# Optimization experiments

Hardware: AMD Instinct MI355X
Metric: run time of the kernel (lower is better)

## Reference

```python
import jax, jax.numpy as jnp
import numpy as np

B, T, H, OUT_STEPS, D = 131072, 51, 64, 20, 4


def setup_inputs() -> dict:
    key = jax.random.key(0)
    ks = jax.random.split(key, 11)
    s = 1.0 / np.sqrt(H)  # torch nn.GRU / nn.Linear uniform init bound
    u = lambda k, shape: jax.random.uniform(k, shape, jnp.float32, -s, s)
    return {
        "input_seq": jax.random.normal(ks[0], (B, T, D), jnp.float32),
        "enc_Wih": u(ks[1], (3 * H, D)),
        "enc_Whh": u(ks[2], (3 * H, H)),
        "enc_bih": u(ks[3], (3 * H,)),
        "enc_bhh": u(ks[4], (3 * H,)),
        "dec_Wih": u(ks[5], (3 * H, D)),
        "dec_Whh": u(ks[6], (3 * H, H)),
        "dec_bih": u(ks[7], (3 * H,)),
        "dec_bhh": u(ks[8], (3 * H,)),
        "lin_W": u(ks[9], (D, H)),
        "lin_b": u(ks[10], (D,)),
    }


def _gru_cell(x, h, Wih, Whh, bih, bhh):
    """PyTorch GRU cell semantics. x: [B,D_in], h: [B,H]."""
    gi = x @ Wih.T + bih  # [B,3H]
    gh = h @ Whh.T + bhh  # [B,3H]
    ir, iz, inn = jnp.split(gi, 3, axis=-1)
    hr, hz, hn = jnp.split(gh, 3, axis=-1)
    r = jax.nn.sigmoid(ir + hr)
    z = jax.nn.sigmoid(iz + hz)
    n = jnp.tanh(inn + r * hn)
    return (1.0 - z) * n + z * h


def reference(input_seq, enc_Wih, enc_Whh, enc_bih, enc_bhh,
              dec_Wih, dec_Whh, dec_bih, dec_bhh, lin_W, lin_b):
    # offset: last observed point, broadcast over the 20 output steps
    offset = input_seq[:, -1:, :]  # [B,1,D]
    diffs = input_seq[:, 1:] - input_seq[:, :-1]  # [B,T-1,D]; dropout p=0 -> identity
    h0 = jnp.zeros((input_seq.shape[0], H), input_seq.dtype)

    def enc_step(h, x_t):
        return _gru_cell(x_t, h, enc_Wih, enc_Whh, enc_bih, enc_bhh), None

    hn, _ = jax.lax.scan(enc_step, h0, jnp.swapaxes(diffs, 0, 1))  # final hidden [B,H]

    def dec_step(carry, _):
        h, px = carry
        h = _gru_cell(px, h, dec_Wih, dec_Whh, dec_bih, dec_bhh)
        x = h @ lin_W.T + lin_b + px  # linear + residual
        return (h, x), x

    _, xs = jax.lax.scan(dec_step, (hn, diffs[:, -1]), None, length=OUT_STEPS)
    out = jnp.swapaxes(xs, 0, 1)  # [B,OUT_STEPS,D]
    return out + offset
```

## Files before the change

kernel.cpp:

```cpp
#include <hip/hip_runtime.h>

namespace {

constexpr int kT = 51;
constexpr int kOut = 20;
constexpr float kL2E  = 1.4426950408889634f;
constexpr float kL2E2 = 2.8853900817779268f;

typedef __attribute__((ext_vector_type(8))) short bf16x8;
typedef __attribute__((ext_vector_type(4))) float f32x4;
typedef __attribute__((ext_vector_type(2))) float f32x2;

union FragU {
    bf16x8 v;
    unsigned long long u64[2];
    unsigned int u32[4];
    unsigned short s[8];
};

__device__ __forceinline__ unsigned short f2bf(float x) {
    union { float f; unsigned int u; } v;
    v.f = x;
    unsigned int r = (v.u + 0x7fffu + ((v.u >> 16) & 1u)) >> 16;
    return (unsigned short)r;
}

__device__ __forceinline__ unsigned int packbf(float a, float b) {
    union { float f; unsigned int u; } ua, ub;
    ua.f = a; ub.f = b;
    return __builtin_amdgcn_perm(ub.u + 0x8000u, ua.u + 0x8000u, 0x07060302u);
}

__global__ __launch_bounds__(256, 2) void gru_encdec(
    const float* __restrict__ input,
    const float* __restrict__ eWih, const float* __restrict__ eWhh,
    const float* __restrict__ ebih, const float* __restrict__ ebhh,
    const float* __restrict__ dWih, const float* __restrict__ dWhh,
    const float* __restrict__ dbih, const float* __restrict__ dbhh,
    const float* __restrict__ linW, const float* __restrict__ linb,
    float* __restrict__ out)
{
    __shared__ __align__(16) unsigned short hbuf[2][4][16 * 68];

    const int lane = (int)(threadIdx.x & 63u);
    const int w = (int)(threadIdx.x >> 6u);
    const int q = lane >> 4;
    const int i = lane & 15;
    const bool q0 = (q == 0);
    const long bb = (long)blockIdx.x * 64 + i;

    const float* xrow[4];
#pragma unroll
    for (int g = 0; g < 4; ++g) xrow[g] = input + (bb + 16 * g) * (kT * 4);

    bf16x8 WA[3][2];
    bf16x8 WAUG[3];
    f32x4 bhhn4;
    float hp[4][4];
    bf16x8 bh[4][2];
    float px[4][4];
    const f32x4 z4 = {0.f, 0.f, 0.f, 0.f};
    const bf16x8 zfr = {0, 0, 0, 0, 0, 0, 0, 0};

    auto load_whh = [&](const float* __restrict__ Whh) {
#pragma unroll
        for (int l = 0; l < 3; ++l) {
            const int tau = 4 * l + w;
            const float sc = (l < 2) ? kL2E : kL2E2;
#pragma unroll
            for (int f = 0; f < 2; ++f) {
                const float* ptr = Whh + (tau * 16 + i) * 64 + f * 32 + q * 8;
                FragU fu;
#pragma unroll
                for (int j = 0; j < 8; ++j) fu.s[j] = f2bf(ptr[j] * sc);
                WA[l][f] = fu.v;
            }
        }
    };

    auto load_aug = [&](const float* __restrict__ Wih,
                        const float* __restrict__ bih,
                        const float* __restrict__ bhh) {
#pragma unroll
        for (int l = 0; l < 3; ++l) {
            const int tau = 4 * l + w;
            const float sc = (l < 2) ? kL2E : kL2E2;
            FragU fu;
            fu.u64[0] = 0; fu.u64[1] = 0;
            if (q0) {
                int j = tau * 16 + i;
#pragma unroll
                for (int d = 0; d < 4; ++d) fu.s[d] = f2bf(Wih[j * 4 + d] * sc);
                float bias = (l < 2) ? (bih[j] + bhh[j]) : bih[j];
                fu.s[4] = f2bf(bias * sc);
            }
            WAUG[l] = fu.v;
        }
#pragma unroll
        for (int r = 0; r < 4; ++r)
            bhhn4[r] = bhh[128 + 16 * w + 4 * q + r] * kL2E2;
    };

    auto make_baug = [&](const float* pxv) -> bf16x8 {
        FragU fu;
        fu.u32[0] = packbf(pxv[0], pxv[1]);
        fu.u32[1] = packbf(pxv[2], pxv[3]);
        fu.u32[2] = 0x3f80u;
        fu.u32[3] = 0u;
        return fu.v;
    };

    auto gru_step = [&](int ssel, const bf16x8* ba) {
#pragma unroll
        for (int p = 0; p < 2; ++p) {
            const int g0 = 2 * p, g1 = 2 * p + 1;
            f32x4 R[2], Z[2], Ni[2], Nh[2];
#pragma unroll
            for (int k = 0; k < 2; ++k) {
                const int g = 2 * p + k;
                R[k] = __builtin_amdgcn_mfma_f32_16x16x32_bf16(WAUG[0], ba[g], z4, 0, 0, 0);
                R[k] = __builtin_amdgcn_mfma_f32_16x16x32_bf16(WA[0][0], bh[g][0], R[k], 0, 0, 0);
                R[k] = __builtin_amdgcn_mfma_f32_16x16x32_bf16(WA[0][1], bh[g][1], R[k], 0, 0, 0);
                Z[k] = __builtin_amdgcn_mfma_f32_16x16x32_bf16(WAUG[1], ba[g], z4, 0, 0, 0);
                Z[k] = __builtin_amdgcn_mfma_f32_16x16x32_bf16(WA[1][0], bh[g][0], Z[k], 0, 0, 0);
                Z[k] = __builtin_amdgcn_mfma_f32_16x16x32_bf16(WA[1][1], bh[g][1], Z[k], 0, 0, 0);
                Ni[k] = __builtin_amdgcn_mfma_f32_16x16x32_bf16(WAUG[2], ba[g], z4, 0, 0, 0);
                Nh[k] = __builtin_amdgcn_mfma_f32_16x16x32_bf16(WA[2][0], bh[g][0], bhhn4, 0, 0, 0);
                Nh[k] = __builtin_amdgcn_mfma_f32_16x16x32_bf16(WA[2][1], bh[g][1], Nh[k], 0, 0, 0);
            }
            float hva[4], hvb[4];
            const f32x2 one = {1.f, 1.f};
            const f32x2 m2 = {-2.f, -2.f};
#pragma unroll
            for (int r = 0; r < 4; ++r) {
                f32x2 a = { __builtin_amdgcn_exp2f(-R[0][r]),
                            __builtin_amdgcn_exp2f(-R[1][r]) };
                f32x2 c = { __builtin_amdgcn_exp2f(-Z[0][r]),
                            __builtin_amdgcn_exp2f(-Z[1][r]) };
                f32x2 A = a + one, C = c + one;
                f32x2 P = A * C;
                float rpp = __builtin_amdgcn_rcpf(P.x * P.y);
                f32x2 Ps = {P.y, P.x};
                f32x2 rp = rpp * Ps;
                f32x2 rr = rp * C;
                f32x2 zz = rp * A;
                f32x2 Nh2 = {Nh[0][r], Nh[1][r]};
                f32x2 Ni2 = {Ni[0][r], Ni[1][r]};
                f32x2 p2 = __builtin_elementwise_fma(rr, Nh2, Ni2);
                f32x2 E = { __builtin_amdgcn_exp2f(p2.x),
                            __builtin_amdgcn_exp2f(p2.y) };
                f32x2 D = E + one;
                float rdd = __builtin_amdgcn_rcpf(D.x * D.y);
                f32x2 Ds = {D.y, D.x};
                f32x2 t = rdd * Ds;
                f32x2 n = __builtin_elementwise_fma(t, m2, one);
                f32x2 h = {hp[g0][r], hp[g1][r]};
                f32x2 hv = __builtin_elementwise_fma(zz, h - n, n);
                hp[g0][r] = hv.x; hp[g1][r] = hv.y;
                hva[r] = hv.x;    hvb[r] = hv.y;
            }
            uint2 wva, wvb;
            wva.x = packbf(hva[0], hva[1]); wva.y = packbf(hva[2], hva[3]);
            wvb.x = packbf(hvb[0], hvb[1]); wvb.y = packbf(hvb[2], hvb[3]);
            *(uint2*)&hbuf[ssel][g0][i * 68 + 16 * w + 4 * q] = wva;
            *(uint2*)&hbuf[ssel][g1][i * 68 + 16 * w + 4 * q] = wvb;
        }
        __syncthreads();
#pragma unroll
        for (int g = 0; g < 4; ++g) {
            const unsigned short* hw = hbuf[ssel][g];
            FragU fA, fB;
            fA.u64[0] = *(const unsigned long long*)&hw[i * 68 + 8 * q];
            fA.u64[1] = *(const unsigned long long*)&hw[i * 68 + 8 * q + 4];
            fB.u64[0] = *(const unsigned long long*)&hw[i * 68 + 32 + 8 * q];
            fB.u64[1] = *(const unsigned long long*)&hw[i * 68 + 32 + 8 * q + 4];
            bh[g][0] = fA.v;
            bh[g][1] = fB.v;
        }
    };

#pragma unroll
    for (int g = 0; g < 4; ++g) {
#pragma unroll
        for (int r = 0; r < 4; ++r) hp[g][r] = 0.f;
        bh[g][0] = zfr;
        bh[g][1] = zfr;
    }
    load_whh(eWhh);
    load_aug(eWih, ebih, ebhh);

    float4 xp[4], xn[4];
#pragma unroll
    for (int g = 0; g < 4; ++g) {
        xp[g] = *(const float4*)(xrow[g]);
        xn[g] = *(const float4*)(xrow[g] + 4);
    }
    bf16x8 ba[4];
#pragma unroll 2
    for (int s = 0; s < kT - 1; ++s) {
#pragma unroll
        for (int g = 0; g < 4; ++g) {
            px[g][0] = xn[g].x - xp[g].x; px[g][1] = xn[g].y - xp[g].y;
            px[g][2] = xn[g].z - xp[g].z; px[g][3] = xn[g].w - xp[g].w;
            xp[g] = xn[g];
        }
        int idx = s + 2; if (idx > kT - 1) idx = kT - 1;
#pragma unroll
        for (int g = 0; g < 4; ++g)
            xn[g] = *(const float4*)(xrow[g] + idx * 4);
#pragma unroll
        for (int g = 0; g < 4; ++g) ba[g] = make_baug(px[g]);
        gru_step(s & 1, ba);
    }
    float4 off[4];
#pragma unroll
    for (int g = 0; g < 4; ++g) off[g] = xp[g];

    load_whh(dWhh);
    load_aug(dWih, dbih, dbhh);

    bf16x8 AL0, AL1, AL2;
    {
        FragU a0, a1, a2;
        a0.u64[0] = a0.u64[1] = 0;
        a1.u64[0] = a1.u64[1] = 0;
        a2.u64[0] = a2.u64[1] = 0;
        if (i < 4) {
            const float* p0 = linW + i * 64 + q * 8;
            const float* p1 = linW + i * 64 + 32 + q * 8;
#pragma unroll
            for (int j = 0; j < 8; ++j) {
                a0.s[j] = f2bf(p0[j]);
                a1.s[j] = f2bf(p1[j]);
            }
            if (q0) a2.s[4] = f2bf(linb[i]);
        }
        AL0 = a0.v; AL1 = a1.v; AL2 = a2.v;
    }

#pragma unroll 2
    for (int s = 0; s < kOut; ++s) {
#pragma unroll
        for (int g = 0; g < 4; ++g) ba[g] = make_baug(px[g]);
        gru_step(s & 1, ba);
#pragma unroll
        for (int g = 0; g < 4; ++g) {
            f32x4 X = __builtin_amdgcn_mfma_f32_16x16x32_bf16(AL2, ba[g], z4, 0, 0, 0);
            X = __builtin_amdgcn_mfma_f32_16x16x32_bf16(AL0, bh[g][0], X, 0, 0, 0);
            X = __builtin_amdgcn_mfma_f32_16x16x32_bf16(AL1, bh[g][1], X, 0, 0, 0);
            px[g][0] += X[0]; px[g][1] += X[1];
            px[g][2] += X[2]; px[g][3] += X[3];
        }
#pragma unroll
        for (int g = 0; g < 4; ++g) {
            if (w == g && q0) {
                float* op = out + (bb + 16 * g) * (kOut * 4) + s * 4;
                float4 v;
                v.x = px[g][0] + off[g].x; v.y = px[g][1] + off[g].y;
                v.z = px[g][2] + off[g].z; v.w = px[g][3] + off[g].w;
                *(float4*)op = v;
            }
        }
    }
}

}

extern "C" void kernel_launch(void* const* d_in, const int* in_sizes, int n_in,
                              void* d_out, int out_size, void* d_ws, size_t ws_size,
                              hipStream_t stream) {
    const float* input = (const float*)d_in[0];
    const float* eWih = (const float*)d_in[1];
    const float* eWhh = (const float*)d_in[2];
    const float* ebih = (const float*)d_in[3];
    const float* ebhh = (const float*)d_in[4];
    const float* dWih = (const float*)d_in[5];
    const float* dWhh = (const float*)d_in[6];
    const float* dbih = (const float*)d_in[7];
    const float* dbhh = (const float*)d_in[8];
    const float* linW = (const float*)d_in[9];
    const float* linb = (const float*)d_in[10];
    float* out = (float*)d_out;

    const int B = in_sizes[0] / (kT * 4);
    const int nblocks = B / 64;
    gru_encdec<<<nblocks, 256, 0, stream>>>(input, eWih, eWhh, ebih, ebhh,
                                            dWih, dWhh, dbih, dbhh,
                                            linW, linb, out);
}
```

Measured before the change: 639.1 us.

## Give each wave its own 16 sequences and keep hidden state in registers

Work is now split by sequence instead of by gate rows: each wave owns 16 batch rows and holds all three gates' weight tiles (12x2 fragments), so it computes every hidden unit itself. The Whh rows are permuted so that the MFMA output layout matches the B-operand layout of the next step. The new hidden state can then be packed straight into bh0/bh1 with no LDS round trip or __syncthreads per timestep. The cost is much higher VGPR use for weights, which with launch_bounds(256,2) may cause spills or lower occupancy, and there are fewer independent MFMA chains per wave to hide latency.

```diff
diff --git a/kernel.cpp b/kernel.cpp
--- a/kernel.cpp
+++ b/kernel.cpp
@@ -40,40 +40,38 @@
     const float* __restrict__ linW, const float* __restrict__ linb,
     float* __restrict__ out)
 {
-    __shared__ __align__(16) unsigned short hbuf[2][4][16 * 68];
-
     const int lane = (int)(threadIdx.x & 63u);
     const int w = (int)(threadIdx.x >> 6u);
     const int q = lane >> 4;
     const int i = lane & 15;
     const bool q0 = (q == 0);
-    const long bb = (long)blockIdx.x * 64 + i;
-
-    const float* xrow[4];
-#pragma unroll
-    for (int g = 0; g < 4; ++g) xrow[g] = input + (bb + 16 * g) * (kT * 4);
-
-    bf16x8 WA[3][2];
-    bf16x8 WAUG[3];
-    f32x4 bhhn4;
+    const long bb = ((long)blockIdx.x * 4 + w) * 16 + i;
+    const float* __restrict__ xrow = input + bb * (kT * 4);
+    const int ibase = 8 * (i >> 2) + (i & 3);
+
+    bf16x8 WA[3][4][2];
+    bf16x8 WAUG[3][4];
+    f32x4 bhhn[4];
     float hp[4][4];
-    bf16x8 bh[4][2];
-    float px[4][4];
+    bf16x8 bh0, bh1;
+    float px[4];
     const f32x4 z4 = {0.f, 0.f, 0.f, 0.f};
-    const bf16x8 zfr = {0, 0, 0, 0, 0, 0, 0, 0};
 
     auto load_whh = [&](const float* __restrict__ Whh) {
 #pragma unroll
         for (int l = 0; l < 3; ++l) {
-            const int tau = 4 * l + w;
             const float sc = (l < 2) ? kL2E : kL2E2;
 #pragma unroll
-            for (int f = 0; f < 2; ++f) {
-                const float* ptr = Whh + (tau * 16 + i) * 64 + f * 32 + q * 8;
-                FragU fu;
-#pragma unroll
-                for (int j = 0; j < 8; ++j) fu.s[j] = f2bf(ptr[j] * sc);
-                WA[l][f] = fu.v;
+            for (int t = 0; t < 4; ++t) {
+                const int rowu = 32 * (t >> 1) + 4 * (t & 1) + ibase;
+#pragma unroll
+                for (int f = 0; f < 2; ++f) {
+                    const float* ptr = Whh + (l * 64 + rowu) * 64 + f * 32 + q * 8;
+                    FragU fu;
+#pragma unroll
+                    for (int j = 0; j < 8; ++j) fu.s[j] = f2bf(ptr[j] * sc);
+                    WA[l][t][f] = fu.v;
+                }
             }
         }
     };
@@ -83,60 +81,61 @@
                         const float* __restrict__ bhh) {
 #pragma unroll
         for (int l = 0; l < 3; ++l) {
-            const int tau = 4 * l + w;
             const float sc = (l < 2) ? kL2E : kL2E2;
-            FragU fu;
-            fu.u64[0] = 0; fu.u64[1] = 0;
-            if (q0) {
-                int j = tau * 16 + i;
-#pragma unroll
-                for (int d = 0; d < 4; ++d) fu.s[d] = f2bf(Wih[j * 4 + d] * sc);
-                float bias = (l < 2) ? (bih[j] + bhh[j]) : bih[j];
-                fu.s[4] = f2bf(bias * sc);
-            }
-            WAUG[l] = fu.v;
-        }
-#pragma unroll
-        for (int r = 0; r < 4; ++r)
-            bhhn4[r] = bhh[128 + 16 * w + 4 * q + r] * kL2E2;
-    };
-
-    auto make_baug = [&](const float* pxv) -> bf16x8 {
+#pragma unroll
+            for (int t = 0; t < 4; ++t) {
+                const int rowu = 32 * (t >> 1) + 4 * (t & 1) + ibase;
+                FragU fu;
+                fu.u64[0] = 0; fu.u64[1] = 0;
+                if (q0) {
+                    int j = l * 64 + rowu;
+#pragma unroll
+                    for (int d = 0; d < 4; ++d) fu.s[d] = f2bf(Wih[j * 4 + d] * sc);
+                    float bias = (l < 2) ? (bih[j] + bhh[j]) : bih[j];
+                    fu.s[4] = f2bf(bias * sc);
+                }
+                WAUG[l][t] = fu.v;
+            }
+        }
+#pragma unroll
+        for (int t = 0; t < 4; ++t) {
+            const int cu = 32 * (t >> 1) + 4 * (t & 1) + 8 * q;
+#pragma unroll
+            for (int r = 0; r < 4; ++r)
+                bhhn[t][r] = bhh[128 + cu + r] * kL2E2;
+        }
+    };
+
+    auto make_baug = [&]() -> bf16x8 {
         FragU fu;
-        fu.u32[0] = packbf(pxv[0], pxv[1]);
-        fu.u32[1] = packbf(pxv[2], pxv[3]);
+        fu.u32[0] = packbf(px[0], px[1]);
+        fu.u32[1] = packbf(px[2], px[3]);
         fu.u32[2] = 0x3f80u;
         fu.u32[3] = 0u;
         return fu.v;
     };
 
-    auto gru_step = [&](int ssel, const bf16x8* ba) {
-#pragma unroll
-        for (int p = 0; p < 2; ++p) {
-            const int g0 = 2 * p, g1 = 2 * p + 1;
-            f32x4 R[2], Z[2], Ni[2], Nh[2];
-#pragma unroll
-            for (int k = 0; k < 2; ++k) {
-                const int g = 2 * p + k;
-                R[k] = __builtin_amdgcn_mfma_f32_16x16x32_bf16(WAUG[0], ba[g], z4, 0, 0, 0);
-                R[k] = __builtin_amdgcn_mfma_f32_16x16x32_bf16(WA[0][0], bh[g][0], R[k], 0, 0, 0);
-                R[k] = __builtin_amdgcn_mfma_f32_16x16x32_bf16(WA[0][1], bh[g][1], R[k], 0, 0, 0);
-                Z[k] = __builtin_amdgcn_mfma_f32_16x16x32_bf16(WAUG[1], ba[g], z4, 0, 0, 0);
-                Z[k] = __builtin_amdgcn_mfma_f32_16x16x32_bf16(WA[1][0], bh[g][0], Z[k], 0, 0, 0);
-                Z[k] = __builtin_amdgcn_mfma_f32_16x16x32_bf16(WA[1][1], bh[g][1], Z[k], 0, 0, 0);
-                Ni[k] = __builtin_amdgcn_mfma_f32_16x16x32_bf16(WAUG[2], ba[g], z4, 0, 0, 0);
-                Nh[k] = __builtin_amdgcn_mfma_f32_16x16x32_bf16(WA[2][0], bh[g][0], bhhn4, 0, 0, 0);
-                Nh[k] = __builtin_amdgcn_mfma_f32_16x16x32_bf16(WA[2][1], bh[g][1], Nh[k], 0, 0, 0);
-            }
-            float hva[4], hvb[4];
-            const f32x2 one = {1.f, 1.f};
-            const f32x2 m2 = {-2.f, -2.f};
-#pragma unroll
-            for (int r = 0; r < 4; ++r) {
-                f32x2 a = { __builtin_amdgcn_exp2f(-R[0][r]),
-                            __builtin_amdgcn_exp2f(-R[1][r]) };
-                f32x2 c = { __builtin_amdgcn_exp2f(-Z[0][r]),
-                            __builtin_amdgcn_exp2f(-Z[1][r]) };
+    auto gru_step = [&](bf16x8 ba) {
+        unsigned int nf[8];
+        const f32x2 one = {1.f, 1.f};
+        const f32x2 m2 = {-2.f, -2.f};
+#pragma unroll
+        for (int t = 0; t < 4; ++t) {
+            f32x4 R = __builtin_amdgcn_mfma_f32_16x16x32_bf16(WAUG[0][t], ba, z4, 0, 0, 0);
+            R = __builtin_amdgcn_mfma_f32_16x16x32_bf16(WA[0][t][0], bh0, R, 0, 0, 0);
+            R = __builtin_amdgcn_mfma_f32_16x16x32_bf16(WA[0][t][1], bh1, R, 0, 0, 0);
+            f32x4 Z = __builtin_amdgcn_mfma_f32_16x16x32_bf16(WAUG[1][t], ba, z4, 0, 0, 0);
+            Z = __builtin_amdgcn_mfma_f32_16x16x32_bf16(WA[1][t][0], bh0, Z, 0, 0, 0);
+            Z = __builtin_amdgcn_mfma_f32_16x16x32_bf16(WA[1][t][1], bh1, Z, 0, 0, 0);
+            f32x4 Ni = __builtin_amdgcn_mfma_f32_16x16x32_bf16(WAUG[2][t], ba, z4, 0, 0, 0);
+            f32x4 Nh = __builtin_amdgcn_mfma_f32_16x16x32_bf16(WA[2][t][0], bh0, bhhn[t], 0, 0, 0);
+            Nh = __builtin_amdgcn_mfma_f32_16x16x32_bf16(WA[2][t][1], bh1, Nh, 0, 0, 0);
+#pragma unroll
+            for (int u = 0; u < 2; ++u) {
+                f32x2 a = { __builtin_amdgcn_exp2f(-R[2 * u]),
+                            __builtin_amdgcn_exp2f(-R[2 * u + 1]) };
+                f32x2 c = { __builtin_amdgcn_exp2f(-Z[2 * u]),
+                            __builtin_amdgcn_exp2f(-Z[2 * u + 1]) };
                 f32x2 A = a + one, C = c + one;
                 f32x2 P = A * C;
                 float rpp = __builtin_amdgcn_rcpf(P.x * P.y);
@@ -144,77 +143,50 @@
                 f32x2 rp = rpp * Ps;
                 f32x2 rr = rp * C;
                 f32x2 zz = rp * A;
-                f32x2 Nh2 = {Nh[0][r], Nh[1][r]};
-                f32x2 Ni2 = {Ni[0][r], Ni[1][r]};
+                f32x2 Nh2 = {Nh[2 * u], Nh[2 * u + 1]};
+                f32x2 Ni2 = {Ni[2 * u], Ni[2 * u + 1]};
                 f32x2 p2 = __builtin_elementwise_fma(rr, Nh2, Ni2);
                 f32x2 E = { __builtin_amdgcn_exp2f(p2.x),
                             __builtin_amdgcn_exp2f(p2.y) };
                 f32x2 D = E + one;
                 float rdd = __builtin_amdgcn_rcpf(D.x * D.y);
                 f32x2 Ds = {D.y, D.x};
-                f32x2 t = rdd * Ds;
-                f32x2 n = __builtin_elementwise_fma(t, m2, one);
-                f32x2 h = {hp[g0][r], hp[g1][r]};
+                f32x2 tt = rdd * Ds;
+                f32x2 n = __builtin_elementwise_fma(tt, m2, one);
+                f32x2 h = {hp[t][2 * u], hp[t][2 * u + 1]};
                 f32x2 hv = __builtin_elementwise_fma(zz, h - n, n);
-                hp[g0][r] = hv.x; hp[g1][r] = hv.y;
-                hva[r] = hv.x;    hvb[r] = hv.y;
-            }
-            uint2 wva, wvb;
-            wva.x = packbf(hva[0], hva[1]); wva.y = packbf(hva[2], hva[3]);
-            wvb.x = packbf(hvb[0], hvb[1]); wvb.y = packbf(hvb[2], hvb[3]);
-            *(uint2*)&hbuf[ssel][g0][i * 68 + 16 * w + 4 * q] = wva;
-            *(uint2*)&hbuf[ssel][g1][i * 68 + 16 * w + 4 * q] = wvb;
-        }
-        __syncthreads();
-#pragma unroll
-        for (int g = 0; g < 4; ++g) {
-            const unsigned short* hw = hbuf[ssel][g];
-            FragU fA, fB;
-            fA.u64[0] = *(const unsigned long long*)&hw[i * 68 + 8 * q];
-            fA.u64[1] = *(const unsigned long long*)&hw[i * 68 + 8 * q + 4];
-            fB.u64[0] = *(const unsigned long long*)&hw[i * 68 + 32 + 8 * q];
-            fB.u64[1] = *(const unsigned long long*)&hw[i * 68 + 32 + 8 * q + 4];
-            bh[g][0] = fA.v;
-            bh[g][1] = fB.v;
-        }
-    };
-
-#pragma unroll
-    for (int g = 0; g < 4; ++g) {
-#pragma unroll
-        for (int r = 0; r < 4; ++r) hp[g][r] = 0.f;
-        bh[g][0] = zfr;
-        bh[g][1] = zfr;
+                hp[t][2 * u] = hv.x; hp[t][2 * u + 1] = hv.y;
+                nf[2 * t + u] = packbf(hv.x, hv.y);
+            }
+        }
+        FragU f0, f1;
+        f0.u32[0] = nf[0]; f0.u32[1] = nf[1]; f0.u32[2] = nf[2]; f0.u32[3] = nf[3];
+        f1.u32[0] = nf[4]; f1.u32[1] = nf[5]; f1.u32[2] = nf[6]; f1.u32[3] = nf[7];
+        bh0 = f0.v; bh1 = f1.v;
+    };
+
+    {
+        const bf16x8 zfr = {0, 0, 0, 0, 0, 0, 0, 0};
+        bh0 = zfr; bh1 = zfr;
+#pragma unroll
+        for (int t = 0; t < 4; ++t)
+#pragma unroll
+            for (int r = 0; r < 4; ++r) hp[t][r] = 0.f;
     }
     load_whh(eWhh);
     load_aug(eWih, ebih, ebhh);
 
-    float4 xp[4], xn[4];
-#pragma unroll
-    for (int g = 0; g < 4; ++g) {
-        xp[g] = *(const float4*)(xrow[g]);
-        xn[g] = *(const float4*)(xrow[g] + 4);
-    }
-    bf16x8 ba[4];
-#pragma unroll 2
+    float4 xp = *(const float4*)(xrow);
+    float4 xn = *(const float4*)(xrow + 4);
     for (int s = 0; s < kT - 1; ++s) {
-#pragma unroll
-        for (int g = 0; g < 4; ++g) {
-            px[g][0] = xn[g].x - xp[g].x; px[g][1] = xn[g].y - xp[g].y;
-            px[g][2] = xn[g].z - xp[g].z; px[g][3] = xn[g].w - xp[g].w;
-            xp[g] = xn[g];
-        }
+        px[0] = xn.x - xp.x; px[1] = xn.y - xp.y;
+        px[2] = xn.z - xp.z; px[3] = xn.w - xp.w;
+        xp = xn;
         int idx = s + 2; if (idx > kT - 1) idx = kT - 1;
-#pragma unroll
-        for (int g = 0; g < 4; ++g)
-            xn[g] = *(const float4*)(xrow[g] + idx * 4);
-#pragma unroll
-        for (int g = 0; g < 4; ++g) ba[g] = make_baug(px[g]);
-        gru_step(s & 1, ba);
-    }
-    float4 off[4];
-#pragma unroll
-    for (int g = 0; g < 4; ++g) off[g] = xp[g];
+        xn = *(const float4*)(xrow + idx * 4);
+        gru_step(make_baug());
+    }
+    const float4 off = xp;
 
     load_whh(dWhh);
     load_aug(dWih, dbih, dbhh);
@@ -238,28 +210,19 @@
         AL0 = a0.v; AL1 = a1.v; AL2 = a2.v;
     }
 
-#pragma unroll 2
+    float* __restrict__ orow = out + bb * (kOut * 4);
     for (int s = 0; s < kOut; ++s) {
-#pragma unroll
-        for (int g = 0; g < 4; ++g) ba[g] = make_baug(px[g]);
-        gru_step(s & 1, ba);
-#pragma unroll
-        for (int g = 0; g < 4; ++g) {
-            f32x4 X = __builtin_amdgcn_mfma_f32_16x16x32_bf16(AL2, ba[g], z4, 0, 0, 0);
-            X = __builtin_amdgcn_mfma_f32_16x16x32_bf16(AL0, bh[g][0], X, 0, 0, 0);
-            X = __builtin_amdgcn_mfma_f32_16x16x32_bf16(AL1, bh[g][1], X, 0, 0, 0);
-            px[g][0] += X[0]; px[g][1] += X[1];
-            px[g][2] += X[2]; px[g][3] += X[3];
-        }
-#pragma unroll
-        for (int g = 0; g < 4; ++g) {
-            if (w == g && q0) {
-                float* op = out + (bb + 16 * g) * (kOut * 4) + s * 4;
-                float4 v;
-                v.x = px[g][0] + off[g].x; v.y = px[g][1] + off[g].y;
-                v.z = px[g][2] + off[g].z; v.w = px[g][3] + off[g].w;
-                *(float4*)op = v;
-            }
+        bf16x8 ba = make_baug();
+        gru_step(ba);
+        f32x4 X = __builtin_amdgcn_mfma_f32_16x16x32_bf16(AL2, ba, z4, 0, 0, 0);
+        X = __builtin_amdgcn_mfma_f32_16x16x32_bf16(AL0, bh0, X, 0, 0, 0);
+        X = __builtin_amdgcn_mfma_f32_16x16x32_bf16(AL1, bh1, X, 0, 0, 0);
+        px[0] += X[0]; px[1] += X[1]; px[2] += X[2]; px[3] += X[3];
+        if (q0) {
+            float4 v;
+            v.x = px[0] + off.x; v.y = px[1] + off.y;
+            v.z = px[2] + off.z; v.w = px[3] + off.w;
+            *(float4*)(orow + s * 4) = v;
         }
     }
 }
```

Measured after the change: 901.0 us. 41.0% more time.
